# Kernel optimization log

Measured on AMD Instinct MI355X. Metric: run time of the kernel, lower is better.

Reference implementation:

```python
import jax, jax.numpy as jnp
import numpy as np

N_HEADS = 16
HID_DIM = 64
INPUT_DIM = 1024
B, L = 4, 1024
NEG = -10000000000.0


def setup_inputs() -> dict:
    key = jax.random.key(0)
    ks = jax.random.split(key, 10)
    d = INPUT_DIM
    h = N_HEADS * HID_DIM
    s = 1.0 / np.sqrt(d)
    return {
        "query": jax.random.normal(ks[0], (B, L, d), dtype=jnp.float32),
        "key": jax.random.normal(ks[1], (B, L, d), dtype=jnp.float32),
        "value": jax.random.normal(ks[2], (B, L, d), dtype=jnp.float32),
        "mask": jax.random.randint(ks[3], (B, 1, L, L), 0, 2, dtype=jnp.int32),
        "wq": jax.random.normal(ks[4], (d, h), dtype=jnp.float32) * s,
        "bq": jnp.zeros((h,), dtype=jnp.float32),
        "wk": jax.random.normal(ks[5], (d, h), dtype=jnp.float32) * s,
        "bk": jnp.zeros((h,), dtype=jnp.float32),
        "wv": jax.random.normal(ks[6], (d, h), dtype=jnp.float32) * s,
        "bv": jnp.zeros((h,), dtype=jnp.float32),
    }


def _split_heads(x):
    # [B, L, H*D] -> [B, H, L, D]
    b, l, _ = x.shape
    return x.reshape(b, l, N_HEADS, HID_DIM).transpose(0, 2, 1, 3)


def reference(query, key, value, mask, wq, bq, wk, bk, wv, bv):
    scale = jnp.sqrt(jnp.float32(HID_DIM))
    Q = _split_heads(query @ wq + bq)   # [B,H,L,D]
    K = _split_heads(key @ wk + bk)
    V = _split_heads(value @ wv + bv)
    energy = jnp.einsum("bhqd,bhkd->bhqk", Q, K) / scale
    energy = jnp.where(mask == 0, jnp.float32(NEG), energy)
    attention = energy  # NOTE: softmax is intentionally skipped, as in the source
    x = jnp.einsum("bhqk,bhkd->bhqd", attention, V)
    x = x.transpose(0, 2, 1, 3).reshape(query.shape[0], -1, N_HEADS * HID_DIM)
    return (attention, x)
```

## Files before the change

kernel.cpp:

```cpp
#include <hip/hip_runtime.h>
#include <stdint.h>
#include <stddef.h>


typedef __attribute__((ext_vector_type(8))) short short8;
typedef __attribute__((ext_vector_type(4))) float f32x4;
typedef __attribute__((ext_vector_type(4))) int i32x4;
typedef __attribute__((ext_vector_type(2))) unsigned int u32x2;

#define MFMA16(a, b, c) __builtin_amdgcn_mfma_f32_16x16x32_bf16(a, b, c, 0, 0, 0)

using gptr_t = const __attribute__((address_space(1))) void*;
using lptr_t = __attribute__((address_space(3))) void*;

#define NEGV -10000000000.0f
#define NEGV_BF16 0xD015u

__device__ __forceinline__ unsigned short f2bf(float f) {
  uint32_t u = __builtin_bit_cast(uint32_t, f);
  u += 0x7FFFu + ((u >> 16) & 1u);
  return (unsigned short)(u >> 16);
}

__global__ __launch_bounds__(256) void k_convert(
    const float* __restrict__ q, const float* __restrict__ k, const float* __restrict__ v,
    unsigned short* __restrict__ oq, unsigned short* __restrict__ ok,
    unsigned short* __restrict__ ov) {
  const int z = blockIdx.z;
  const float* src = z == 0 ? q : z == 1 ? k : v;
  unsigned short* dst = z == 0 ? oq : z == 1 ? ok : ov;
  const size_t idx = ((size_t)blockIdx.x * 256 + threadIdx.x) * 8;
  f32x4 a = *(const f32x4*)(src + idx);
  f32x4 b = *(const f32x4*)(src + idx + 4);
  short8 o;
  o[0] = (short)f2bf(a[0]); o[1] = (short)f2bf(a[1]);
  o[2] = (short)f2bf(a[2]); o[3] = (short)f2bf(a[3]);
  o[4] = (short)f2bf(b[0]); o[5] = (short)f2bf(b[1]);
  o[6] = (short)f2bf(b[2]); o[7] = (short)f2bf(b[3]);
  *(short8*)(dst + idx) = o;
}

__global__ __launch_bounds__(256) void k_wt(
    const float* __restrict__ wq, const float* __restrict__ wk, const float* __restrict__ wv,
    unsigned short* __restrict__ tq, unsigned short* __restrict__ tk,
    unsigned short* __restrict__ tv) {
  const int z = blockIdx.z;
  const float* src = z == 0 ? wq : z == 1 ? wk : wv;
  unsigned short* dst = z == 0 ? tq : z == 1 ? tk : tv;
  __shared__ unsigned short t[64][65];
  const int n0 = blockIdx.x * 64, k0 = blockIdx.y * 64;
#pragma unroll
  for (int i = 0; i < 16; ++i) {
    const int idx = i * 256 + threadIdx.x;
    const int r = idx >> 6, c = idx & 63;
    t[r][c] = f2bf(src[(size_t)(k0 + r) * 1024 + n0 + c]);
  }
  __syncthreads();
#pragma unroll
  for (int i = 0; i < 16; ++i) {
    const int idx = i * 256 + threadIdx.x;
    const int r = idx >> 6, c = idx & 63;
    dst[(size_t)(n0 + r) * 1024 + k0 + c] = t[c][r];
  }
}

__global__ __launch_bounds__(256) void k_gemm(
    const unsigned short* __restrict__ Xq, const unsigned short* __restrict__ Xk,
    const unsigned short* __restrict__ Xv,
    const unsigned short* __restrict__ Wq, const unsigned short* __restrict__ Wk,
    const unsigned short* __restrict__ Wv,
    const float* __restrict__ bq, const float* __restrict__ bk, const float* __restrict__ bv,
    unsigned short* __restrict__ Cq, unsigned short* __restrict__ Ck,
    unsigned short* __restrict__ Vt) {
  const int bid = blockIdx.x;
  const int wg = (bid & 7) * 96 + (bid >> 3);
  const int z = wg >> 8, rem = wg & 255;
  const unsigned short* X  = z == 0 ? Xq : z == 1 ? Xk : Xv;
  const unsigned short* Wt = z == 0 ? Wq : z == 1 ? Wk : Wv;
  const float* bias        = z == 0 ? bq : z == 1 ? bk : bv;

  __shared__ unsigned short Ads[128 * 64];
  __shared__ unsigned short Bds[128 * 64];

  const int tid = threadIdx.x;
  const int w = tid >> 6, l = tid & 63;
  const int lr = l & 15, g = l >> 4;
  const int m0 = (rem >> 3) * 128, n0 = (rem & 7) * 128;
  const int wm = (w >> 1) * 64, wn = (w & 1) * 64;
  const int srow = tid >> 3, sslot = tid & 7;

  f32x4 acc[4][4];
#pragma unroll
  for (int mi = 0; mi < 4; ++mi)
#pragma unroll
    for (int ni = 0; ni < 4; ++ni) acc[mi][ni] = (f32x4){0.f, 0.f, 0.f, 0.f};

  for (int kt = 0; kt < 16; ++kt) {
    const int kb = kt * 64;
#pragma unroll
    for (int i = 0; i < 4; ++i) {
      const int row = i * 32 + srow;
      const int scol = ((sslot ^ (row & 7)) << 3);
      const unsigned short* ga = X + (size_t)(m0 + row) * 1024 + kb + scol;
      const unsigned short* gb = Wt + (size_t)(n0 + row) * 1024 + kb + scol;
      __builtin_amdgcn_global_load_lds((gptr_t)ga, (lptr_t)&Ads[(i * 32 + w * 8) * 64], 16, 0, 0);
      __builtin_amdgcn_global_load_lds((gptr_t)gb, (lptr_t)&Bds[(i * 32 + w * 8) * 64], 16, 0, 0);
    }
    __syncthreads();
    short8 afr[4][2], bfr[4][2];
#pragma unroll
    for (int t = 0; t < 4; ++t)
#pragma unroll
      for (int ks = 0; ks < 2; ++ks) {
        const int ra = wm + t * 16 + lr;
        afr[t][ks] = *(const short8*)&Ads[ra * 64 + (((ks * 4 + g) ^ (ra & 7)) << 3)];
        const int rb = wn + t * 16 + lr;
        bfr[t][ks] = *(const short8*)&Bds[rb * 64 + (((ks * 4 + g) ^ (rb & 7)) << 3)];
      }
#pragma unroll
    for (int ks = 0; ks < 2; ++ks)
#pragma unroll
      for (int mi = 0; mi < 4; ++mi)
#pragma unroll
        for (int ni = 0; ni < 4; ++ni)
          acc[mi][ni] = MFMA16(afr[mi][ks], bfr[ni][ks], acc[mi][ni]);
    __syncthreads();
  }

  if (z != 2) {
    unsigned short* C = z == 0 ? Cq : Ck;
#pragma unroll
    for (int mi = 0; mi < 4; ++mi)
#pragma unroll
      for (int ni = 0; ni < 4; ++ni) {
        const int n = n0 + wn + ni * 16 + lr;
        const float bs = bias[n];
        f32x4 a = acc[mi][ni];
#pragma unroll
        for (int r = 0; r < 4; ++r) {
          const int m = m0 + wm + mi * 16 + g * 4 + r;
          C[(size_t)m * 1024 + n] = f2bf(a[r] + bs);
        }
      }
  } else {
#pragma unroll
    for (int mi = 0; mi < 4; ++mi)
#pragma unroll
      for (int ni = 0; ni < 4; ++ni) {
        const int ng = n0 + wn + ni * 16 + lr;
        const int hh = ng >> 6, dd = ng & 63;
        const float bs = bias[ng];
        f32x4 a = acc[mi][ni];
        const int mg = m0 + wm + mi * 16 + g * 4;
        const int bb = mg >> 10, ll = mg & 1023;
        u32x2 pk;
        pk[0] = (uint32_t)f2bf(a[0] + bs) | ((uint32_t)f2bf(a[1] + bs) << 16);
        pk[1] = (uint32_t)f2bf(a[2] + bs) | ((uint32_t)f2bf(a[3] + bs) << 16);
        *(u32x2*)&Vt[(size_t)((bb * 16 + hh) * 64 + dd) * 1024 + ll] = pk;
      }
  }
}

__global__ __launch_bounds__(512, 6) void k_attn(
    const unsigned short* __restrict__ Qb, const unsigned short* __restrict__ Kb,
    const unsigned short* __restrict__ Vt, const int* __restrict__ mask,
    float* __restrict__ att, float* __restrict__ xout) {
  const int bid = blockIdx.x;
  const int wg = (bid & 7) * 64 + (bid >> 3);
  const int bh = wg >> 3, qt = wg & 7;
  const int b = bh >> 4, h = bh & 15;
  const int tid = threadIdx.x;
  const int w = tid >> 6, l = tid & 63;
  const int lr = l & 15, g = l >> 4;
  const int q0 = qt * 128 + w * 16;

  __shared__ unsigned short Kl[128 * 64];
  __shared__ unsigned short Vl[64 * 128];
  __shared__ unsigned short Pl[8][16 * 64];
  unsigned short* Pw = Pl[w];

  short8 qf[2];
#pragma unroll
  for (int ks = 0; ks < 2; ++ks)
    qf[ks] = *(const short8*)&Qb[(size_t)(b * 1024 + q0 + lr) * 1024 +
                                 h * 64 + ks * 32 + g * 8];

  f32x4 xacc[4];
#pragma unroll
  for (int di = 0; di < 4; ++di) xacc[di] = (f32x4){0.f, 0.f, 0.f, 0.f};

  for (int kt = 0; kt < 8; ++kt) {
    const int kb = kt * 128;
    __syncthreads();
#pragma unroll
    for (int i = 0; i < 2; ++i) {
      const int row = i * 64 + (tid >> 3);
      const int slot = tid & 7;
      const unsigned short* src = Kb + (size_t)(b * 1024 + kb + row) * 1024 +
                                  h * 64 + ((slot ^ (row & 7)) << 3);
      __builtin_amdgcn_global_load_lds((gptr_t)src, (lptr_t)&Kl[(i * 64 + w * 8) * 64], 16, 0, 0);
    }
#pragma unroll
    for (int i = 0; i < 2; ++i) {
      const int row = i * 32 + (tid >> 4);
      const int slot = tid & 15;
      const unsigned short* src = Vt + (size_t)(bh * 64 + row) * 1024 + kb +
                                  ((slot ^ (row & 7)) << 3);
      __builtin_amdgcn_global_load_lds((gptr_t)src, (lptr_t)&Vl[(i * 32 + w * 4) * 128], 16, 0, 0);
    }
    __syncthreads();

#pragma unroll
    for (int h2 = 0; h2 < 2; ++h2) {
      f32x4 s[4];
#pragma unroll
      for (int n2 = 0; n2 < 4; ++n2) {
        const int row = (h2 * 4 + n2) * 16 + lr;
        f32x4 a = (f32x4){0.f, 0.f, 0.f, 0.f};
#pragma unroll
        for (int ks = 0; ks < 2; ++ks) {
          short8 kf = *(const short8*)&Kl[row * 64 + (((ks * 4 + g) ^ (row & 7)) << 3)];
          a = MFMA16(kf, qf[ks], a);
        }
        s[n2] = a;
      }
#pragma unroll
      for (int n2 = 0; n2 < 4; ++n2) {
        u32x2 pk;
        pk[0] = (uint32_t)f2bf(s[n2][0] * 0.125f) | ((uint32_t)f2bf(s[n2][1] * 0.125f) << 16);
        pk[1] = (uint32_t)f2bf(s[n2][2] * 0.125f) | ((uint32_t)f2bf(s[n2][3] * 0.125f) << 16);
        const int c16 = n2 * 2 + (g >> 1);
        *(u32x2*)&Pw[lr * 64 + ((c16 ^ (lr & 7)) << 3) + (g & 1) * 4] = pk;
      }
      asm volatile("s_waitcnt lgkmcnt(0)" ::: "memory");
      __builtin_amdgcn_sched_barrier(0);
#pragma unroll
      for (int p = 0; p < 4; ++p) {
        const int row = p * 4 + g;
        const int col = lr * 4;
        const int eb = row * 64 + (((lr >> 1) ^ (row & 7)) << 3) + (lr & 1) * 4;
        u32x2 pr = *(const u32x2*)&Pw[eb];
        i32x4 mv = *(const i32x4*)&mask[(size_t)(b * 1024 + q0 + row) * 1024 +
                                        kb + h2 * 64 + col];
        const uint32_t u0 = pr[0], u1 = pr[1];
        f32x4 e;
        e[0] = mv[0] ? __builtin_bit_cast(float, u0 << 16) : NEGV;
        e[1] = mv[1] ? __builtin_bit_cast(float, u0 & 0xFFFF0000u) : NEGV;
        e[2] = mv[2] ? __builtin_bit_cast(float, u1 << 16) : NEGV;
        e[3] = mv[3] ? __builtin_bit_cast(float, u1 & 0xFFFF0000u) : NEGV;
        __builtin_nontemporal_store(
            e, (f32x4*)&att[(size_t)(bh * 1024 + q0 + row) * 1024 + kb + h2 * 64 + col]);
        u32x2 wb;
        wb[0] = (mv[0] ? (u0 & 0xFFFFu) : NEGV_BF16) |
                ((mv[1] ? (u0 >> 16) : NEGV_BF16) << 16);
        wb[1] = (mv[2] ? (u1 & 0xFFFFu) : NEGV_BF16) |
                ((mv[3] ? (u1 >> 16) : NEGV_BF16) << 16);
        *(u32x2*)&Pw[eb] = wb;
      }
      asm volatile("s_waitcnt lgkmcnt(0)" ::: "memory");
      __builtin_amdgcn_sched_barrier(0);
#pragma unroll
      for (int k2 = 0; k2 < 2; ++k2) {
        const int c16 = k2 * 4 + g;
        short8 pa = *(const short8*)&Pw[lr * 64 + ((c16 ^ (lr & 7)) << 3)];
        const int colk = h2 * 64 + k2 * 32 + g * 8;
#pragma unroll
        for (int di = 0; di < 4; ++di) {
          const int vr = di * 16 + lr;
          short8 vf = *(const short8*)&Vl[vr * 128 + (colk ^ ((vr & 7) << 3))];
          xacc[di] = MFMA16(pa, vf, xacc[di]);
        }
      }
      asm volatile("" ::: "memory");
    }
  }

#pragma unroll
  for (int di = 0; di < 4; ++di) {
    f32x4 a = xacc[di];
#pragma unroll
    for (int r = 0; r < 4; ++r) {
      const int q = q0 + g * 4 + r;
      __builtin_nontemporal_store(
          a[r], &xout[(size_t)(b * 1024 + q) * 1024 + h * 64 + di * 16 + lr]);
    }
  }
}

extern "C" void kernel_launch(void* const* d_in, const int* in_sizes, int n_in,
                              void* d_out, int out_size, void* d_ws, size_t ws_size,
                              hipStream_t stream) {
  (void)in_sizes; (void)n_in; (void)out_size;
  const float* q   = (const float*)d_in[0];
  const float* k   = (const float*)d_in[1];
  const float* v   = (const float*)d_in[2];
  const int* mask  = (const int*)d_in[3];
  const float* wq  = (const float*)d_in[4];
  const float* bq  = (const float*)d_in[5];
  const float* wk  = (const float*)d_in[6];
  const float* bk  = (const float*)d_in[7];
  const float* wv  = (const float*)d_in[8];
  const float* bv  = (const float*)d_in[9];
  float* att = (float*)d_out;
  float* x   = att + (size_t)4 * 16 * 1024 * 1024;

  char* ws = (char*)d_ws;
  const size_t SZX = (size_t)4096 * 1024 * 2;
  const size_t SZW = (size_t)1024 * 1024 * 2;
  if (ws_size < 6 * SZX + 3 * SZW) return;
  unsigned short* Xq  = (unsigned short*)(ws);
  unsigned short* Xk  = (unsigned short*)(ws + SZX);
  unsigned short* Xv  = (unsigned short*)(ws + 2 * SZX);
  unsigned short* Wtq = (unsigned short*)(ws + 3 * SZX);
  unsigned short* Wtk = (unsigned short*)(ws + 3 * SZX + SZW);
  unsigned short* Wtv = (unsigned short*)(ws + 3 * SZX + 2 * SZW);
  unsigned short* Qb  = (unsigned short*)(ws + 3 * SZX + 3 * SZW);
  unsigned short* Kb  = (unsigned short*)(ws + 4 * SZX + 3 * SZW);
  unsigned short* Vt  = (unsigned short*)(ws + 5 * SZX + 3 * SZW);

  k_convert<<<dim3(2048, 1, 3), 256, 0, stream>>>(q, k, v, Xq, Xk, Xv);
  k_wt<<<dim3(16, 16, 3), 256, 0, stream>>>(wq, wk, wv, Wtq, Wtk, Wtv);
  k_gemm<<<dim3(768), 256, 0, stream>>>(Xq, Xk, Xv, Wtq, Wtk, Wtv,
                                        bq, bk, bv, Qb, Kb, Vt);
  k_attn<<<dim3(512), 512, 0, stream>>>(Qb, Kb, Vt, mask, att, x);
}
```

Measured before the change: 164.1 us.

## Pack mask into bitmasks and double-buffer K/V tiles in attention kernel

Adds a pre-pass that compresses the int32 mask into 64-bit ballot bitmasks, so the attention kernel reads 1 bit per element instead of 4 bytes per head. The attention loop moves to 64-wide key tiles with double-buffered K/V LDS staging, prefetching the next tile while computing the current one. The mask is now applied before bf16 rounding, which makes the P@V path and the stored attention consistent. The extra launch and the change of grid ordering, which drops the earlier block swizzle, may affect cache locality.

Result: slower. 180.4 us (+9.9%).

```diff
diff --git a/kernel.cpp b/kernel.cpp
--- a/kernel.cpp
+++ b/kernel.cpp
@@ -14,12 +14,24 @@
 using lptr_t = __attribute__((address_space(3))) void*;
 
 #define NEGV -10000000000.0f
-#define NEGV_BF16 0xD015u
 
 __device__ __forceinline__ unsigned short f2bf(float f) {
   uint32_t u = __builtin_bit_cast(uint32_t, f);
   u += 0x7FFFu + ((u >> 16) & 1u);
   return (unsigned short)(u >> 16);
+}
+
+__global__ __launch_bounds__(256) void k_maskpack(const int* __restrict__ mask,
+                                                  unsigned long long* __restrict__ mb) {
+  const int wid = (blockIdx.x * 256 + threadIdx.x) >> 6;
+  const int l = threadIdx.x & 63;
+#pragma unroll 4
+  for (int i = 0; i < 32; ++i) {
+    const size_t c = (size_t)wid * 32 + i;
+    const int v = mask[c * 64 + l];
+    const unsigned long long bits = __ballot(v != 0);
+    if (l == 0) mb[c] = bits;
+  }
 }
 
 __global__ __launch_bounds__(256) void k_convert(
@@ -163,21 +175,33 @@
 
 __global__ __launch_bounds__(512, 6) void k_attn(
     const unsigned short* __restrict__ Qb, const unsigned short* __restrict__ Kb,
-    const unsigned short* __restrict__ Vt, const int* __restrict__ mask,
+    const unsigned short* __restrict__ Vt, const uint32_t* __restrict__ mb,
     float* __restrict__ att, float* __restrict__ xout) {
-  const int bid = blockIdx.x;
-  const int wg = (bid & 7) * 64 + (bid >> 3);
-  const int bh = wg >> 3, qt = wg & 7;
-  const int b = bh >> 4, h = bh & 15;
+  const int bh = blockIdx.y, b = bh >> 4, h = bh & 15;
   const int tid = threadIdx.x;
   const int w = tid >> 6, l = tid & 63;
   const int lr = l & 15, g = l >> 4;
-  const int q0 = qt * 128 + w * 16;
-
-  __shared__ unsigned short Kl[128 * 64];
-  __shared__ unsigned short Vl[64 * 128];
+  const int q0 = blockIdx.x * 128 + w * 16;
+
+  __shared__ unsigned short Kl[2][64 * 64];
+  __shared__ unsigned short Vl[2][64 * 64];
   __shared__ unsigned short Pl[8][16 * 64];
   unsigned short* Pw = Pl[w];
+
+  const int srow = tid >> 3, sslot = tid & 7;
+  const int scol = ((sslot ^ (srow & 7)) << 3);
+
+#define STAGE(t, bb)                                                            \
+  do {                                                                          \
+    const unsigned short* sk = Kb + (size_t)(b * 1024 + (t) * 64 + srow) * 1024 \
+                               + h * 64 + scol;                                 \
+    __builtin_amdgcn_global_load_lds((gptr_t)sk, (lptr_t)&Kl[bb][(w * 8) * 64], \
+                                     16, 0, 0);                                 \
+    const unsigned short* sv = Vt + (size_t)(bh * 64 + srow) * 1024 +           \
+                               (t) * 64 + scol;                                 \
+    __builtin_amdgcn_global_load_lds((gptr_t)sv, (lptr_t)&Vl[bb][(w * 8) * 64], \
+                                     16, 0, 0);                                 \
+  } while (0)
 
   short8 qf[2];
 #pragma unroll
@@ -189,91 +213,86 @@
 #pragma unroll
   for (int di = 0; di < 4; ++di) xacc[di] = (f32x4){0.f, 0.f, 0.f, 0.f};
 
-  for (int kt = 0; kt < 8; ++kt) {
-    const int kb = kt * 128;
-    __syncthreads();
-#pragma unroll
-    for (int i = 0; i < 2; ++i) {
-      const int row = i * 64 + (tid >> 3);
-      const int slot = tid & 7;
-      const unsigned short* src = Kb + (size_t)(b * 1024 + kb + row) * 1024 +
-                                  h * 64 + ((slot ^ (row & 7)) << 3);
-      __builtin_amdgcn_global_load_lds((gptr_t)src, (lptr_t)&Kl[(i * 64 + w * 8) * 64], 16, 0, 0);
-    }
-#pragma unroll
-    for (int i = 0; i < 2; ++i) {
-      const int row = i * 32 + (tid >> 4);
-      const int slot = tid & 15;
-      const unsigned short* src = Vt + (size_t)(bh * 64 + row) * 1024 + kb +
-                                  ((slot ^ (row & 7)) << 3);
-      __builtin_amdgcn_global_load_lds((gptr_t)src, (lptr_t)&Vl[(i * 32 + w * 4) * 128], 16, 0, 0);
-    }
-    __syncthreads();
-
-#pragma unroll
-    for (int h2 = 0; h2 < 2; ++h2) {
-      f32x4 s[4];
-#pragma unroll
-      for (int n2 = 0; n2 < 4; ++n2) {
-        const int row = (h2 * 4 + n2) * 16 + lr;
-        f32x4 a = (f32x4){0.f, 0.f, 0.f, 0.f};
-#pragma unroll
-        for (int ks = 0; ks < 2; ++ks) {
-          short8 kf = *(const short8*)&Kl[row * 64 + (((ks * 4 + g) ^ (row & 7)) << 3)];
-          a = MFMA16(kf, qf[ks], a);
-        }
-        s[n2] = a;
-      }
-#pragma unroll
-      for (int n2 = 0; n2 < 4; ++n2) {
-        u32x2 pk;
-        pk[0] = (uint32_t)f2bf(s[n2][0] * 0.125f) | ((uint32_t)f2bf(s[n2][1] * 0.125f) << 16);
-        pk[1] = (uint32_t)f2bf(s[n2][2] * 0.125f) | ((uint32_t)f2bf(s[n2][3] * 0.125f) << 16);
-        const int c16 = n2 * 2 + (g >> 1);
-        *(u32x2*)&Pw[lr * 64 + ((c16 ^ (lr & 7)) << 3) + (g & 1) * 4] = pk;
-      }
-      asm volatile("s_waitcnt lgkmcnt(0)" ::: "memory");
+  const size_t brow = (size_t)(b * 1024 + q0 + lr) * 32;
+
+  STAGE(0, 0);
+  u32x2 bitsc = *(const u32x2*)&mb[brow];
+  asm volatile("s_waitcnt vmcnt(0)" ::: "memory");
+  __builtin_amdgcn_s_barrier();
+  __builtin_amdgcn_sched_barrier(0);
+
+  for (int kt = 0; kt < 16; ++kt) {
+    const int cur = kt & 1;
+    u32x2 bitsn = bitsc;
+    if (kt < 15) {
+      STAGE(kt + 1, cur ^ 1);
+      bitsn = *(const u32x2*)&mb[brow + (kt + 1) * 2];
+    }
+
+    f32x4 s[4];
+#pragma unroll
+    for (int n2 = 0; n2 < 4; ++n2) {
+      const int row = n2 * 16 + lr;
+      f32x4 a = (f32x4){0.f, 0.f, 0.f, 0.f};
+#pragma unroll
+      for (int ks = 0; ks < 2; ++ks) {
+        short8 kf = *(const short8*)&Kl[cur][row * 64 + (((ks * 4 + g) ^ (row & 7)) << 3)];
+        a = MFMA16(kf, qf[ks], a);
+      }
+      s[n2] = a;
+    }
+#pragma unroll
+    for (int n2 = 0; n2 < 4; ++n2) {
+      const uint32_t wbits = bitsc[n2 >> 1];
+      const int bit0 = (n2 & 1) * 16 + g * 4;
+      f32x4 e;
+#pragma unroll
+      for (int j = 0; j < 4; ++j)
+        e[j] = ((wbits >> (bit0 + j)) & 1u) ? s[n2][j] * 0.125f : NEGV;
+      u32x2 pk;
+      pk[0] = (uint32_t)f2bf(e[0]) | ((uint32_t)f2bf(e[1]) << 16);
+      pk[1] = (uint32_t)f2bf(e[2]) | ((uint32_t)f2bf(e[3]) << 16);
+      const int c16 = n2 * 2 + (g >> 1);
+      *(u32x2*)&Pw[lr * 64 + ((c16 ^ (lr & 7)) << 3) + (g & 1) * 4] = pk;
+    }
+    asm volatile("s_waitcnt lgkmcnt(0)" ::: "memory");
+    __builtin_amdgcn_sched_barrier(0);
+#pragma unroll
+    for (int p = 0; p < 4; ++p) {
+      const int row = p * 4 + g;
+      const int eb = row * 64 + (((lr >> 1) ^ (row & 7)) << 3) + (lr & 1) * 4;
+      u32x2 pr = *(const u32x2*)&Pw[eb];
+      const uint32_t u0 = pr[0], u1 = pr[1];
+      f32x4 e;
+      e[0] = __builtin_bit_cast(float, u0 << 16);
+      e[1] = __builtin_bit_cast(float, u0 & 0xFFFF0000u);
+      e[2] = __builtin_bit_cast(float, u1 << 16);
+      e[3] = __builtin_bit_cast(float, u1 & 0xFFFF0000u);
+      __builtin_nontemporal_store(
+          e, (f32x4*)&att[(size_t)(bh * 1024 + q0 + row) * 1024 + kt * 64 + lr * 4]);
+    }
+#pragma unroll
+    for (int k2 = 0; k2 < 2; ++k2) {
+      const int c16 = k2 * 4 + g;
+      short8 pa = *(const short8*)&Pw[lr * 64 + ((c16 ^ (lr & 7)) << 3)];
+      const int colk = k2 * 32 + g * 8;
+#pragma unroll
+      for (int di = 0; di < 4; ++di) {
+        const int vr = di * 16 + lr;
+        short8 vf = *(const short8*)&Vl[cur][vr * 64 + (colk ^ ((vr & 7) << 3))];
+        xacc[di] = MFMA16(pa, vf, xacc[di]);
+      }
+    }
+    asm volatile("" ::: "memory");
+
+    bitsc = bitsn;
+    if (kt < 15) {
+      asm volatile("s_waitcnt vmcnt(5)" ::: "memory");
+      __builtin_amdgcn_s_barrier();
       __builtin_amdgcn_sched_barrier(0);
-#pragma unroll
-      for (int p = 0; p < 4; ++p) {
-        const int row = p * 4 + g;
-        const int col = lr * 4;
-        const int eb = row * 64 + (((lr >> 1) ^ (row & 7)) << 3) + (lr & 1) * 4;
-        u32x2 pr = *(const u32x2*)&Pw[eb];
-        i32x4 mv = *(const i32x4*)&mask[(size_t)(b * 1024 + q0 + row) * 1024 +
-                                        kb + h2 * 64 + col];
-        const uint32_t u0 = pr[0], u1 = pr[1];
-        f32x4 e;
-        e[0] = mv[0] ? __builtin_bit_cast(float, u0 << 16) : NEGV;
-        e[1] = mv[1] ? __builtin_bit_cast(float, u0 & 0xFFFF0000u) : NEGV;
-        e[2] = mv[2] ? __builtin_bit_cast(float, u1 << 16) : NEGV;
-        e[3] = mv[3] ? __builtin_bit_cast(float, u1 & 0xFFFF0000u) : NEGV;
-        __builtin_nontemporal_store(
-            e, (f32x4*)&att[(size_t)(bh * 1024 + q0 + row) * 1024 + kb + h2 * 64 + col]);
-        u32x2 wb;
-        wb[0] = (mv[0] ? (u0 & 0xFFFFu) : NEGV_BF16) |
-                ((mv[1] ? (u0 >> 16) : NEGV_BF16) << 16);
-        wb[1] = (mv[2] ? (u1 & 0xFFFFu) : NEGV_BF16) |
-                ((mv[3] ? (u1 >> 16) : NEGV_BF16) << 16);
-        *(u32x2*)&Pw[eb] = wb;
-      }
-      asm volatile("s_waitcnt lgkmcnt(0)" ::: "memory");
-      __builtin_amdgcn_sched_barrier(0);
-#pragma unroll
-      for (int k2 = 0; k2 < 2; ++k2) {
-        const int c16 = k2 * 4 + g;
-        short8 pa = *(const short8*)&Pw[lr * 64 + ((c16 ^ (lr & 7)) << 3)];
-        const int colk = h2 * 64 + k2 * 32 + g * 8;
-#pragma unroll
-        for (int di = 0; di < 4; ++di) {
-          const int vr = di * 16 + lr;
-          short8 vf = *(const short8*)&Vl[vr * 128 + (colk ^ ((vr & 7) << 3))];
-          xacc[di] = MFMA16(pa, vf, xacc[di]);
-        }
-      }
-      asm volatile("" ::: "memory");
-    }
-  }
+    }
+  }
+#undef STAGE
 
 #pragma unroll
   for (int di = 0; di < 4; ++di) {
@@ -307,7 +326,8 @@
   char* ws = (char*)d_ws;
   const size_t SZX = (size_t)4096 * 1024 * 2;
   const size_t SZW = (size_t)1024 * 1024 * 2;
-  if (ws_size < 6 * SZX + 3 * SZW) return;
+  const size_t SZM = (size_t)4 * 1024 * 16 * 8;
+  if (ws_size < 6 * SZX + 3 * SZW + SZM) return;
   unsigned short* Xq  = (unsigned short*)(ws);
   unsigned short* Xk  = (unsigned short*)(ws + SZX);
   unsigned short* Xv  = (unsigned short*)(ws + 2 * SZX);
@@ -317,10 +337,13 @@
   unsigned short* Qb  = (unsigned short*)(ws + 3 * SZX + 3 * SZW);
   unsigned short* Kb  = (unsigned short*)(ws + 4 * SZX + 3 * SZW);
   unsigned short* Vt  = (unsigned short*)(ws + 5 * SZX + 3 * SZW);
-
+  unsigned long long* Mb = (unsigned long long*)(ws + 6 * SZX + 3 * SZW);
+
+  k_maskpack<<<dim3(512), 256, 0, stream>>>(mask, Mb);
   k_convert<<<dim3(2048, 1, 3), 256, 0, stream>>>(q, k, v, Xq, Xk, Xv);
   k_wt<<<dim3(16, 16, 3), 256, 0, stream>>>(wq, wk, wv, Wtq, Wtk, Wtv);
   k_gemm<<<dim3(768), 256, 0, stream>>>(Xq, Xk, Xv, Wtq, Wtk, Wtv,
                                         bq, bk, bv, Qb, Kb, Vt);
-  k_attn<<<dim3(512), 512, 0, stream>>>(Qb, Kb, Vt, mask, att, x);
-}
+  k_attn<<<dim3(8, 64), 512, 0, stream>>>(Qb, Kb, Vt, (const uint32_t*)Mb,
+                                          att, x);
+}
```
